# Optimization experiments

Measured on AMD Instinct MI355X. Metric: run time of the kernel, lower is better.

## Reference

```python
import jax, jax.numpy as jnp
import numpy as np

N = 50000
E = 800000
D = 128
EPS = 1e-12


def setup_inputs() -> dict:
    key = jax.random.key(0)
    ks = jax.random.split(key, 16)
    s = 1.0 / np.sqrt(D)
    inp = {
        "x": jax.random.normal(ks[0], (N, D), dtype=jnp.float32),
        "edge_src": jax.random.randint(ks[1], (E,), 0, N, dtype=jnp.int32),
        "edge_dst": jax.random.randint(ks[2], (E,), 0, N, dtype=jnp.int32),
    }
    names = ["Wpool0", "Wself0", "Wneigh0", "Wpool1", "Wself1", "Wneigh1"]
    for i, n in enumerate(names):
        inp[n] = jax.random.uniform(ks[3 + i], (D, D), dtype=jnp.float32, minval=-s, maxval=s)
    for i, n in enumerate(["bpool0", "b0", "bpool1", "b1"]):
        inp[n] = jax.random.uniform(ks[9 + i], (D,), dtype=jnp.float32, minval=-s, maxval=s)
    return inp


def _sage_pool(h, src, dst, Wpool, bpool, Wself, Wneigh, b):
    # per-neighbor transform: relu(fc_pool(h_src))
    m = jax.nn.relu(h @ Wpool.T + bpool)            # [N, D]
    # gather -> segment max over destination nodes (irregular access)
    agg = jax.ops.segment_max(m[src], dst, num_segments=N)  # [N, D], -inf for empty
    deg = jax.ops.segment_sum(jnp.ones((E,), jnp.float32), dst, num_segments=N)
    h_neigh = jnp.where(deg[:, None] > 0, agg, 0.0)  # DGL: zero for isolated nodes
    return h @ Wself.T + h_neigh @ Wneigh.T + b


def _l2norm(h):
    # torch F.normalize(dim=1, eps=1e-12)
    n = jnp.sqrt(jnp.sum(h * h, axis=1, keepdims=True))
    return h / jnp.maximum(n, EPS)


def reference(x, edge_src, edge_dst,
              Wpool0, Wself0, Wneigh0, Wpool1, Wself1, Wneigh1,
              bpool0, b0, bpool1, b1):
    # layer 0 (not last): conv -> relu -> normalize -> dropout(p=0)
    h = _sage_pool(x, edge_src, edge_dst, Wpool0, bpool0, Wself0, Wneigh0, b0)
    h = jax.nn.relu(h)
    h = _l2norm(h)
    enc_feat_input = h  # l == n_layers - 2
    # layer 1 (last): conv only
    h = _sage_pool(h, edge_src, edge_dst, Wpool1, bpool1, Wself1, Wneigh1, b1)
    return h, enc_feat_input
```

## Files before the change

kernel.cpp:

```cpp
#include <hip/hip_runtime.h>
#include <hip/hip_fp16.h>

#define DD 128
#define BK_SHIFT 6
#define BK_NODES 64
#define NBLK 256
#define SCAN_T 1024
#define SCAN_E 8
#define SCAN_CHUNK (SCAN_T * SCAN_E)

typedef __attribute__((ext_vector_type(8))) _Float16 f16x8;
typedef __attribute__((ext_vector_type(4))) float f32x4;

union h8u { f16x8 v; int i[4]; };

static __device__ __forceinline__ f16x8 vmax8(f16x8 a, f16x8 b) {
#pragma unroll
    for (int i = 0; i < 8; ++i) a[i] = a[i] > b[i] ? a[i] : b[i];
    return a;
}

__global__ void prep_w(const float* __restrict__ W0, const float* __restrict__ W1,
                       const float* __restrict__ W2, const float* __restrict__ W3,
                       const float* __restrict__ W4, const float* __restrict__ W5,
                       __half* __restrict__ Wh) {
    int idx = blockIdx.x * 256 + threadIdx.x;
    int wi = idx >> 14;
    int off = idx & 16383;
    int j = off >> 7;
    int k = off & 127;
    float a;
    switch (wi) {
        case 0: a = W0[off]; break;
        case 1: a = W1[off]; break;
        case 2: a = W2[off]; break;
        case 3: a = W3[off]; break;
        case 4: a = W4[off]; break;
        default: a = W5[off]; break;
    }
    int k2 = k ^ ((j & 7) << 3);
    Wh[(size_t)wi * 16384 + j * DD + k2] = __float2half(a);
}

__global__ void prep_x(const float* __restrict__ x, __half* __restrict__ xh, int n8) {
    int i = blockIdx.x * 256 + threadIdx.x;
    if (i >= n8) return;
    float4 u0 = *(const float4*)(x + (size_t)i * 8);
    float4 u1 = *(const float4*)(x + (size_t)i * 8 + 4);
    f16x8 v;
    v[0] = (_Float16)u0.x; v[1] = (_Float16)u0.y; v[2] = (_Float16)u0.z; v[3] = (_Float16)u0.w;
    v[4] = (_Float16)u1.x; v[5] = (_Float16)u1.y; v[6] = (_Float16)u1.z; v[7] = (_Float16)u1.w;
    *(f16x8*)(xh + (size_t)i * 8) = v;
}

__global__ __launch_bounds__(256) void hist2d_kernel(const int* __restrict__ dst,
                                                     int* __restrict__ hist2d,
                                                     int E, int NB, int chunk) {
    extern __shared__ int h[];
    int t = threadIdx.x, b = blockIdx.x;
    for (int i = t; i < NB; i += 256) h[i] = 0;
    __syncthreads();
    int e0 = b * chunk, e1 = min(e0 + chunk, E);
    for (int e = e0 + t; e < e1; e += 256)
        atomicAdd(&h[dst[e] >> BK_SHIFT], 1);
    __syncthreads();
    for (int i = t; i < NB; i += 256) hist2d[i * NBLK + b] = h[i];
}

__global__ __launch_bounds__(SCAN_T) void partial_reduce(const int* __restrict__ data,
                                                         int* __restrict__ bsum, int n) {
    __shared__ int s[SCAN_T];
    int t = threadIdx.x;
    int i0 = blockIdx.x * SCAN_CHUNK + t * SCAN_E;
    int sum = 0;
#pragma unroll
    for (int u = 0; u < SCAN_E; ++u) {
        int i = i0 + u;
        sum += (i < n) ? data[i] : 0;
    }
    s[t] = sum;
    __syncthreads();
    for (int off = SCAN_T / 2; off > 0; off >>= 1) {
        if (t < off) s[t] += s[t + off];
        __syncthreads();
    }
    if (t == 0) bsum[blockIdx.x] = s[0];
}

__global__ __launch_bounds__(SCAN_T) void scan_excl_inplace(int* __restrict__ data,
                                                            const int* __restrict__ bsum, int n) {
    __shared__ int s[SCAN_T];
    int t = threadIdx.x;
    int b = blockIdx.x;
    int carry = 0;
    for (int k = 0; k < b; ++k) carry += bsum[k];
    int i0 = b * SCAN_CHUNK + t * SCAN_E;
    int v[SCAN_E];
    int sum = 0;
#pragma unroll
    for (int u = 0; u < SCAN_E; ++u) {
        v[u] = (i0 + u < n) ? data[i0 + u] : 0;
        sum += v[u];
    }
    s[t] = sum;
    __syncthreads();
    for (int off = 1; off < SCAN_T; off <<= 1) {
        int x = (t >= off) ? s[t - off] : 0;
        __syncthreads();
        s[t] += x;
        __syncthreads();
    }
    int run = s[t] - sum + carry;
#pragma unroll
    for (int u = 0; u < SCAN_E; ++u) {
        int i = i0 + u;
        if (i < n) {
            data[i] = run;
            run += v[u];
        }
    }
}

__global__ __launch_bounds__(256) void bin_edges2(const int* __restrict__ src,
                                                  const int* __restrict__ dst,
                                                  const int* __restrict__ base,
                                                  unsigned* __restrict__ ebuf,
                                                  int E, int NB, int chunk) {
    extern __shared__ int h[];
    int t = threadIdx.x, b = blockIdx.x;
    for (int i = t; i < NB; i += 256) h[i] = base[i * NBLK + b];
    __syncthreads();
    int e0 = b * chunk, e1 = min(e0 + chunk, E);
    for (int e = e0 + t; e < e1; e += 256) {
        int d = dst[e];
        int p = atomicAdd(&h[d >> BK_SHIFT], 1);
        ebuf[p] = ((unsigned)src[e] << BK_SHIFT) | (unsigned)(d & (BK_NODES - 1));
    }
}

__global__ __launch_bounds__(256) void build_csr(const unsigned* __restrict__ ebuf,
                                                 const int* __restrict__ base,
                                                 int* __restrict__ rowptr,
                                                 int* __restrict__ csr_src, int N, int NB, int E) {
    __shared__ int cnt[BK_NODES];
    __shared__ int cur[BK_NODES];
    int b = blockIdx.x;
    int t = threadIdx.x;
    int beg = base[b * NBLK];
    int end = (b == NB - 1) ? E : base[(b + 1) * NBLK];
    if (b == 0 && t == 0) rowptr[0] = 0;
    if (t < BK_NODES) cnt[t] = 0;
    __syncthreads();
    for (int e = beg + t; e < end; e += 256)
        atomicAdd(&cnt[ebuf[e] & (BK_NODES - 1)], 1);
    __syncthreads();
    if (t < 64) {
        int v = cnt[t];
        int inc = v;
#pragma unroll
        for (int off = 1; off < 64; off <<= 1) {
            int x = __shfl_up(inc, off);
            if (t >= off) inc += x;
        }
        cur[t] = beg + inc - v;
        int node = b * BK_NODES + t;
        if (node < N) rowptr[node + 1] = beg + inc;
    }
    __syncthreads();
    for (int e = beg + t; e < end; e += 256) {
        unsigned v = ebuf[e];
        int p = atomicAdd(&cur[v & (BK_NODES - 1)], 1);
        csr_src[p] = (int)(v >> BK_SHIFT);
    }
}

__global__ __launch_bounds__(256) void segmax2(const __half* __restrict__ m,
                                               const int* __restrict__ rowptr,
                                               const int* __restrict__ csr_src,
                                               __half* __restrict__ agg, int n) {
    int node = blockIdx.x * 4 + (threadIdx.x >> 6);
    if (node >= n) return;
    int lane = threadIdx.x & 63;
    int g = lane >> 4;
    int l = lane & 15;
    int beg = rowptr[node], end = rowptr[node + 1];
    const __half* mp = m + l * 8;

    f16x8 acc0 = (f16x8)0, acc1 = (f16x8)0, acc2 = (f16x8)0, acc3 = (f16x8)0;

    int e = beg + g;
    for (; e + 12 < end; e += 16) {
        int s0 = csr_src[e];
        int s1 = csr_src[e + 4];
        int s2 = csr_src[e + 8];
        int s3 = csr_src[e + 12];
        f16x8 u0 = *(const f16x8*)(mp + (size_t)s0 * DD);
        f16x8 u1 = *(const f16x8*)(mp + (size_t)s1 * DD);
        f16x8 u2 = *(const f16x8*)(mp + (size_t)s2 * DD);
        f16x8 u3 = *(const f16x8*)(mp + (size_t)s3 * DD);
        acc0 = vmax8(acc0, u0);
        acc1 = vmax8(acc1, u1);
        acc2 = vmax8(acc2, u2);
        acc3 = vmax8(acc3, u3);
    }
    for (; e < end; e += 4) {
        int s0 = csr_src[e];
        f16x8 u0 = *(const f16x8*)(mp + (size_t)s0 * DD);
        acc0 = vmax8(acc0, u0);
    }

    h8u a;
    a.v = vmax8(vmax8(acc0, acc1), vmax8(acc2, acc3));
#pragma unroll
    for (int off = 16; off <= 32; off <<= 1) {
        h8u b;
#pragma unroll
        for (int c = 0; c < 4; ++c) b.i[c] = __shfl_xor(a.i[c], off);
        a.v = vmax8(a.v, b.v);
    }
    if (g == 0)
        *(f16x8*)(agg + (size_t)node * DD + l * 8) = a.v;
}

template <int EPI, bool FUSED>
__global__ __launch_bounds__(256) void gemm_f16(
    const __half* __restrict__ A,
    const __half* __restrict__ WA,
    const __half* __restrict__ G,
    const __half* __restrict__ WG,
    const float* __restrict__ bias,
    float* __restrict__ outf, __half* __restrict__ outh, int nrows) {
    __shared__ __half Ws[DD * DD];
    int tid = threadIdx.x;
    int lane = tid & 63;
    int w = tid >> 6;
    int l16 = lane & 15;
    int lg = lane >> 4;
    int rbase = blockIdx.x * 128 + w * 32;

    {
        const f32x4* src = (const f32x4*)(const void*)WA;
        f32x4* dst = (f32x4*)(void*)Ws;
#pragma unroll
        for (int i = 0; i < 8; ++i) dst[i * 256 + tid] = src[i * 256 + tid];
    }
    __syncthreads();

    int ar0 = min(rbase + l16, nrows - 1);
    int ar1 = min(rbase + 16 + l16, nrows - 1);
    size_t aoff0 = (size_t)ar0 * DD;
    size_t aoff1 = (size_t)ar1 * DD;

    f32x4 acc[2][8];
#pragma unroll
    for (int mt = 0; mt < 2; ++mt)
#pragma unroll
        for (int nt = 0; nt < 8; ++nt) acc[mt][nt] = (f32x4){0.f, 0.f, 0.f, 0.f};

    int swz = (l16 & 7) << 3;

#pragma unroll
    for (int kk = 0; kk < 4; ++kk) {
        int k0 = kk * 32 + lg * 8;
        f16x8 a0 = *(const f16x8*)(const void*)(A + aoff0 + k0);
        f16x8 a1 = *(const f16x8*)(const void*)(A + aoff1 + k0);
        int klds = k0 ^ swz;
#pragma unroll
        for (int nt = 0; nt < 8; ++nt) {
            f16x8 wh = *(const f16x8*)(const void*)(Ws + (nt * 16 + l16) * DD + klds);
            acc[0][nt] = __builtin_amdgcn_mfma_f32_16x16x32_f16(a0, wh, acc[0][nt], 0, 0, 0);
            acc[1][nt] = __builtin_amdgcn_mfma_f32_16x16x32_f16(a1, wh, acc[1][nt], 0, 0, 0);
        }
    }

    if constexpr (FUSED) {
        __syncthreads();
        {
            const f32x4* src = (const f32x4*)(const void*)WG;
            f32x4* dst = (f32x4*)(void*)Ws;
#pragma unroll
            for (int i = 0; i < 8; ++i) dst[i * 256 + tid] = src[i * 256 + tid];
        }
        __syncthreads();
#pragma unroll
        for (int kk = 0; kk < 4; ++kk) {
            int k0 = kk * 32 + lg * 8;
            f16x8 g0 = *(const f16x8*)(const void*)(G + aoff0 + k0);
            f16x8 g1 = *(const f16x8*)(const void*)(G + aoff1 + k0);
            int klds = k0 ^ swz;
#pragma unroll
            for (int nt = 0; nt < 8; ++nt) {
                f16x8 uh = *(const f16x8*)(const void*)(Ws + (nt * 16 + l16) * DD + klds);
                acc[0][nt] = __builtin_amdgcn_mfma_f32_16x16x32_f16(g0, uh, acc[0][nt], 0, 0, 0);
                acc[1][nt] = __builtin_amdgcn_mfma_f32_16x16x32_f16(g1, uh, acc[1][nt], 0, 0, 0);
            }
        }
    }

    float bv[8];
#pragma unroll
    for (int nt = 0; nt < 8; ++nt) bv[nt] = bias[nt * 16 + l16];

#pragma unroll
    for (int mt = 0; mt < 2; ++mt) {
#pragma unroll
        for (int r = 0; r < 4; ++r) {
            int row = rbase + mt * 16 + lg * 4 + r;
            float vv[8];
            float s = 0.f;
#pragma unroll
            for (int nt = 0; nt < 8; ++nt) {
                float v = acc[mt][nt][r] + bv[nt];
                if (EPI >= 1) v = fmaxf(v, 0.f);
                vv[nt] = v;
                s += v * v;
            }
            if constexpr (EPI == 2) {
                s += __shfl_xor(s, 1);
                s += __shfl_xor(s, 2);
                s += __shfl_xor(s, 4);
                s += __shfl_xor(s, 8);
                float sc = 1.0f / fmaxf(sqrtf(s), 1e-12f);
#pragma unroll
                for (int nt = 0; nt < 8; ++nt) vv[nt] *= sc;
            }
            if (row < nrows) {
                if constexpr (EPI == 1) {
#pragma unroll
                    for (int nt = 0; nt < 8; ++nt)
                        outh[(size_t)row * DD + nt * 16 + l16] = __float2half(vv[nt]);
                } else {
#pragma unroll
                    for (int nt = 0; nt < 8; ++nt)
                        outf[(size_t)row * DD + nt * 16 + l16] = vv[nt];
                    if (EPI == 2 && outh != nullptr) {
#pragma unroll
                        for (int nt = 0; nt < 8; ++nt)
                            outh[(size_t)row * DD + nt * 16 + l16] = __float2half(vv[nt]);
                    }
                }
            }
        }
    }
}

static inline size_t align16(size_t x) { return (x + 15) & ~(size_t)15; }

extern "C" void kernel_launch(void* const* d_in, const int* in_sizes, int n_in,
                              void* d_out, int out_size, void* d_ws, size_t ws_size,
                              hipStream_t stream) {
    const float* x  = (const float*)d_in[0];
    const int* esrc = (const int*)d_in[1];
    const int* edst = (const int*)d_in[2];
    const float* Wm[6];
    for (int i = 0; i < 6; ++i) Wm[i] = (const float*)d_in[3 + i];
    const float* bpool0 = (const float*)d_in[9];
    const float* b0     = (const float*)d_in[10];
    const float* bpool1 = (const float*)d_in[11];
    const float* b1     = (const float*)d_in[12];

    int N = in_sizes[0] / DD;
    int E = in_sizes[1];
    int NB = (N + BK_NODES - 1) >> BK_SHIFT;
    int chunk = (E + NBLK - 1) / NBLK;
    int nh = NB * NBLK;
    int nscan = (nh + SCAN_CHUNK - 1) / SCAN_CHUNK;

    char* p = (char*)d_ws;
    __half* Wh     = (__half*)p;   p += align16((size_t)6 * 16384 * 2);
    __half* xh     = (__half*)p;   p += align16((size_t)N * DD * 2);
    __half* ench   = (__half*)p;   p += align16((size_t)N * DD * 2);
    __half* m      = (__half*)p;   p += align16((size_t)N * DD * 2);
    __half* agg    = (__half*)p;   p += align16((size_t)N * DD * 2);
    int* hist2d    = (int*)p;      p += align16((size_t)nh * 4);
    int* bsum      = (int*)p;      p += align16((size_t)nscan * 4);
    int* rowptr    = (int*)p;      p += align16((size_t)(N + 1) * 4);
    unsigned* ebuf = (unsigned*)p; p += align16((size_t)E * 4);
    int* csr_src   = (int*)p;      p += align16((size_t)E * 4);

    float* out_h   = (float*)d_out;
    float* out_enc = (float*)d_out + (size_t)N * DD;

    prep_w<<<384, 256, 0, stream>>>(Wm[0], Wm[1], Wm[2], Wm[3], Wm[4], Wm[5], Wh);
    prep_x<<<(N * DD / 8 + 255) / 256, 256, 0, stream>>>(x, xh, N * DD / 8);
    hist2d_kernel<<<NBLK, 256, NB * 4, stream>>>(edst, hist2d, E, NB, chunk);
    partial_reduce<<<nscan, SCAN_T, 0, stream>>>(hist2d, bsum, nh);
    scan_excl_inplace<<<nscan, SCAN_T, 0, stream>>>(hist2d, bsum, nh);
    bin_edges2<<<NBLK, 256, NB * 4, stream>>>(esrc, edst, hist2d, ebuf, E, NB, chunk);
    build_csr<<<NB, 256, 0, stream>>>(ebuf, hist2d, rowptr, csr_src, N, NB, E);

    int gb = (N + 127) / 128;
    int sb = (N + 3) / 4;

    gemm_f16<1, false><<<gb, 256, 0, stream>>>(xh, Wh + 0 * 16384, nullptr, nullptr,
                                               bpool0, nullptr, m, N);
    segmax2<<<sb, 256, 0, stream>>>(m, rowptr, csr_src, agg, N);
    gemm_f16<2, true><<<gb, 256, 0, stream>>>(xh, Wh + 1 * 16384, agg, Wh + 2 * 16384,
                                              b0, out_enc, ench, N);

    gemm_f16<1, false><<<gb, 256, 0, stream>>>(ench, Wh + 3 * 16384, nullptr, nullptr,
                                               bpool1, nullptr, m, N);
    segmax2<<<sb, 256, 0, stream>>>(m, rowptr, csr_src, agg, N);
    gemm_f16<0, true><<<gb, 256, 0, stream>>>(ench, Wh + 4 * 16384, agg, Wh + 5 * 16384,
                                              b1, out_h, nullptr, N);
}
```

Before: 173.6 us.

## Split segment-max feature dimension across grid y into four 32-column slices

```diff
diff --git a/kernel.cpp b/kernel.cpp
--- a/kernel.cpp
+++ b/kernel.cpp
@@ -10,13 +10,14 @@
 #define SCAN_CHUNK (SCAN_T * SCAN_E)
 
 typedef __attribute__((ext_vector_type(8))) _Float16 f16x8;
+typedef __attribute__((ext_vector_type(2))) _Float16 f16x2;
 typedef __attribute__((ext_vector_type(4))) float f32x4;
 
-union h8u { f16x8 v; int i[4]; };
-
-static __device__ __forceinline__ f16x8 vmax8(f16x8 a, f16x8 b) {
-#pragma unroll
-    for (int i = 0; i < 8; ++i) a[i] = a[i] > b[i] ? a[i] : b[i];
+union h2u { f16x2 v; int i; };
+
+static __device__ __forceinline__ f16x2 vmax2(f16x2 a, f16x2 b) {
+    a[0] = a[0] > b[0] ? a[0] : b[0];
+    a[1] = a[1] > b[1] ? a[1] : b[1];
     return a;
 }
 
@@ -174,19 +175,20 @@
     }
 }
 
-__global__ __launch_bounds__(256) void segmax2(const __half* __restrict__ m,
-                                               const int* __restrict__ rowptr,
-                                               const int* __restrict__ csr_src,
-                                               __half* __restrict__ agg, int n) {
-    int node = blockIdx.x * 4 + (threadIdx.x >> 6);
+__global__ __launch_bounds__(1024) void segmax3(const __half* __restrict__ m,
+                                                const int* __restrict__ rowptr,
+                                                const int* __restrict__ csr_src,
+                                                __half* __restrict__ agg, int n) {
+    int node = blockIdx.x * 16 + (threadIdx.x >> 6);
     if (node >= n) return;
+    int q = blockIdx.y;
     int lane = threadIdx.x & 63;
     int g = lane >> 4;
     int l = lane & 15;
     int beg = rowptr[node], end = rowptr[node + 1];
-    const __half* mp = m + l * 8;
-
-    f16x8 acc0 = (f16x8)0, acc1 = (f16x8)0, acc2 = (f16x8)0, acc3 = (f16x8)0;
+    const __half* mp = m + q * 32 + l * 2;
+
+    f16x2 a0 = (f16x2)0, a1 = (f16x2)0, a2 = (f16x2)0, a3 = (f16x2)0;
 
     int e = beg + g;
     for (; e + 12 < end; e += 16) {
@@ -194,32 +196,31 @@
         int s1 = csr_src[e + 4];
         int s2 = csr_src[e + 8];
         int s3 = csr_src[e + 12];
-        f16x8 u0 = *(const f16x8*)(mp + (size_t)s0 * DD);
-        f16x8 u1 = *(const f16x8*)(mp + (size_t)s1 * DD);
-        f16x8 u2 = *(const f16x8*)(mp + (size_t)s2 * DD);
-        f16x8 u3 = *(const f16x8*)(mp + (size_t)s3 * DD);
-        acc0 = vmax8(acc0, u0);
-        acc1 = vmax8(acc1, u1);
-        acc2 = vmax8(acc2, u2);
-        acc3 = vmax8(acc3, u3);
+        f16x2 u0 = *(const f16x2*)(mp + (size_t)s0 * DD);
+        f16x2 u1 = *(const f16x2*)(mp + (size_t)s1 * DD);
+        f16x2 u2 = *(const f16x2*)(mp + (size_t)s2 * DD);
+        f16x2 u3 = *(const f16x2*)(mp + (size_t)s3 * DD);
+        a0 = vmax2(a0, u0);
+        a1 = vmax2(a1, u1);
+        a2 = vmax2(a2, u2);
+        a3 = vmax2(a3, u3);
     }
     for (; e < end; e += 4) {
         int s0 = csr_src[e];
-        f16x8 u0 = *(const f16x8*)(mp + (size_t)s0 * DD);
-        acc0 = vmax8(acc0, u0);
-    }
-
-    h8u a;
-    a.v = vmax8(vmax8(acc0, acc1), vmax8(acc2, acc3));
+        f16x2 u0 = *(const f16x2*)(mp + (size_t)s0 * DD);
+        a0 = vmax2(a0, u0);
+    }
+
+    h2u a;
+    a.v = vmax2(vmax2(a0, a1), vmax2(a2, a3));
 #pragma unroll
     for (int off = 16; off <= 32; off <<= 1) {
-        h8u b;
-#pragma unroll
-        for (int c = 0; c < 4; ++c) b.i[c] = __shfl_xor(a.i[c], off);
-        a.v = vmax8(a.v, b.v);
+        h2u b;
+        b.i = __shfl_xor(a.i, off);
+        a.v = vmax2(a.v, b.v);
     }
     if (g == 0)
-        *(f16x8*)(agg + (size_t)node * DD + l * 8) = a.v;
+        *(f16x2*)(agg + (size_t)node * DD + q * 32 + l * 2) = a.v;
 }
 
 template <int EPI, bool FUSED>
@@ -390,17 +391,17 @@
     build_csr<<<NB, 256, 0, stream>>>(ebuf, hist2d, rowptr, csr_src, N, NB, E);
 
     int gb = (N + 127) / 128;
-    int sb = (N + 3) / 4;
+    dim3 sg((N + 15) / 16, 4);
 
     gemm_f16<1, false><<<gb, 256, 0, stream>>>(xh, Wh + 0 * 16384, nullptr, nullptr,
                                                bpool0, nullptr, m, N);
-    segmax2<<<sb, 256, 0, stream>>>(m, rowptr, csr_src, agg, N);
+    segmax3<<<sg, 1024, 0, stream>>>(m, rowptr, csr_src, agg, N);
     gemm_f16<2, true><<<gb, 256, 0, stream>>>(xh, Wh + 1 * 16384, agg, Wh + 2 * 16384,
                                               b0, out_enc, ench, N);
 
     gemm_f16<1, false><<<gb, 256, 0, stream>>>(ench, Wh + 3 * 16384, nullptr, nullptr,
                                                bpool1, nullptr, m, N);
-    segmax2<<<sb, 256, 0, stream>>>(m, rowptr, csr_src, agg, N);
+    segmax3<<<sg, 1024, 0, stream>>>(m, rowptr, csr_src, agg, N);
     gemm_f16<0, true><<<gb, 256, 0, stream>>>(ench, Wh + 4 * 16384, agg, Wh + 5 * 16384,
                                               b1, out_h, nullptr, N);
 }
```

Measured after the change: 278.9 us. 60.6% more time.

## Split GEMM output columns across two wave groups with 512-thread blocks

Applied to the files above, without the earlier changes.

```diff
diff --git a/kernel.cpp b/kernel.cpp
--- a/kernel.cpp
+++ b/kernel.cpp
@@ -223,7 +223,7 @@
 }
 
 template <int EPI, bool FUSED>
-__global__ __launch_bounds__(256) void gemm_f16(
+__global__ __launch_bounds__(512) void gemm_f16(
     const __half* __restrict__ A,
     const __half* __restrict__ WA,
     const __half* __restrict__ G,
@@ -231,18 +231,22 @@
     const float* __restrict__ bias,
     float* __restrict__ outf, __half* __restrict__ outh, int nrows) {
     __shared__ __half Ws[DD * DD];
+    __shared__ float pbuf[2][DD];
     int tid = threadIdx.x;
     int lane = tid & 63;
     int w = tid >> 6;
     int l16 = lane & 15;
     int lg = lane >> 4;
-    int rbase = blockIdx.x * 128 + w * 32;
+    int ch = w >> 2;
+    int wr = w & 3;
+    int blk0 = blockIdx.x * 128;
+    int rbase = blk0 + wr * 32;
 
     {
         const f32x4* src = (const f32x4*)(const void*)WA;
         f32x4* dst = (f32x4*)(void*)Ws;
 #pragma unroll
-        for (int i = 0; i < 8; ++i) dst[i * 256 + tid] = src[i * 256 + tid];
+        for (int i = 0; i < 4; ++i) dst[i * 512 + tid] = src[i * 512 + tid];
     }
     __syncthreads();
 
@@ -251,11 +255,11 @@
     size_t aoff0 = (size_t)ar0 * DD;
     size_t aoff1 = (size_t)ar1 * DD;
 
-    f32x4 acc[2][8];
+    f32x4 acc[2][4];
 #pragma unroll
     for (int mt = 0; mt < 2; ++mt)
 #pragma unroll
-        for (int nt = 0; nt < 8; ++nt) acc[mt][nt] = (f32x4){0.f, 0.f, 0.f, 0.f};
+        for (int nt = 0; nt < 4; ++nt) acc[mt][nt] = (f32x4){0.f, 0.f, 0.f, 0.f};
 
     int swz = (l16 & 7) << 3;
 
@@ -266,8 +270,8 @@
         f16x8 a1 = *(const f16x8*)(const void*)(A + aoff1 + k0);
         int klds = k0 ^ swz;
 #pragma unroll
-        for (int nt = 0; nt < 8; ++nt) {
-            f16x8 wh = *(const f16x8*)(const void*)(Ws + (nt * 16 + l16) * DD + klds);
+        for (int nt = 0; nt < 4; ++nt) {
+            f16x8 wh = *(const f16x8*)(const void*)(Ws + (ch * 64 + nt * 16 + l16) * DD + klds);
             acc[0][nt] = __builtin_amdgcn_mfma_f32_16x16x32_f16(a0, wh, acc[0][nt], 0, 0, 0);
             acc[1][nt] = __builtin_amdgcn_mfma_f32_16x16x32_f16(a1, wh, acc[1][nt], 0, 0, 0);
         }
@@ -279,7 +283,7 @@
             const f32x4* src = (const f32x4*)(const void*)WG;
             f32x4* dst = (f32x4*)(void*)Ws;
 #pragma unroll
-            for (int i = 0; i < 8; ++i) dst[i * 256 + tid] = src[i * 256 + tid];
+            for (int i = 0; i < 4; ++i) dst[i * 512 + tid] = src[i * 512 + tid];
         }
         __syncthreads();
 #pragma unroll
@@ -289,55 +293,70 @@
             f16x8 g1 = *(const f16x8*)(const void*)(G + aoff1 + k0);
             int klds = k0 ^ swz;
 #pragma unroll
-            for (int nt = 0; nt < 8; ++nt) {
-                f16x8 uh = *(const f16x8*)(const void*)(Ws + (nt * 16 + l16) * DD + klds);
+            for (int nt = 0; nt < 4; ++nt) {
+                f16x8 uh = *(const f16x8*)(const void*)(Ws + (ch * 64 + nt * 16 + l16) * DD + klds);
                 acc[0][nt] = __builtin_amdgcn_mfma_f32_16x16x32_f16(g0, uh, acc[0][nt], 0, 0, 0);
                 acc[1][nt] = __builtin_amdgcn_mfma_f32_16x16x32_f16(g1, uh, acc[1][nt], 0, 0, 0);
             }
         }
     }
 
-    float bv[8];
-#pragma unroll
-    for (int nt = 0; nt < 8; ++nt) bv[nt] = bias[nt * 16 + l16];
-
-#pragma unroll
-    for (int mt = 0; mt < 2; ++mt) {
-#pragma unroll
-        for (int r = 0; r < 4; ++r) {
-            int row = rbase + mt * 16 + lg * 4 + r;
-            float vv[8];
-            float s = 0.f;
-#pragma unroll
-            for (int nt = 0; nt < 8; ++nt) {
-                float v = acc[mt][nt][r] + bv[nt];
-                if (EPI >= 1) v = fmaxf(v, 0.f);
-                vv[nt] = v;
-                s += v * v;
-            }
-            if constexpr (EPI == 2) {
+    float bv[4];
+#pragma unroll
+    for (int nt = 0; nt < 4; ++nt) bv[nt] = bias[ch * 64 + nt * 16 + l16];
+
+    if constexpr (EPI == 2) {
+#pragma unroll
+        for (int mt = 0; mt < 2; ++mt) {
+#pragma unroll
+            for (int r = 0; r < 4; ++r) {
+                float s = 0.f;
+#pragma unroll
+                for (int nt = 0; nt < 4; ++nt) {
+                    float v = fmaxf(acc[mt][nt][r] + bv[nt], 0.f);
+                    s += v * v;
+                }
                 s += __shfl_xor(s, 1);
                 s += __shfl_xor(s, 2);
                 s += __shfl_xor(s, 4);
                 s += __shfl_xor(s, 8);
-                float sc = 1.0f / fmaxf(sqrtf(s), 1e-12f);
-#pragma unroll
-                for (int nt = 0; nt < 8; ++nt) vv[nt] *= sc;
+                if (l16 == 0) pbuf[ch][wr * 32 + mt * 16 + lg * 4 + r] = s;
             }
-            if (row < nrows) {
-                if constexpr (EPI == 1) {
-#pragma unroll
-                    for (int nt = 0; nt < 8; ++nt)
-                        outh[(size_t)row * DD + nt * 16 + l16] = __float2half(vv[nt]);
-                } else {
-#pragma unroll
-                    for (int nt = 0; nt < 8; ++nt)
-                        outf[(size_t)row * DD + nt * 16 + l16] = vv[nt];
-                    if (EPI == 2 && outh != nullptr) {
-#pragma unroll
-                        for (int nt = 0; nt < 8; ++nt)
-                            outh[(size_t)row * DD + nt * 16 + l16] = __float2half(vv[nt]);
+        }
+        __syncthreads();
+#pragma unroll
+        for (int mt = 0; mt < 2; ++mt) {
+#pragma unroll
+            for (int r = 0; r < 4; ++r) {
+                int lrow = wr * 32 + mt * 16 + lg * 4 + r;
+                int row = blk0 + lrow;
+                float tot = pbuf[0][lrow] + pbuf[1][lrow];
+                float sc = 1.0f / fmaxf(sqrtf(tot), 1e-12f);
+                if (row < nrows) {
+#pragma unroll
+                    for (int nt = 0; nt < 4; ++nt) {
+                        float v = fmaxf(acc[mt][nt][r] + bv[nt], 0.f) * sc;
+                        size_t o = (size_t)row * DD + ch * 64 + nt * 16 + l16;
+                        outf[o] = v;
+                        outh[o] = __float2half(v);
                     }
+                }
+            }
+        }
+    } else {
+#pragma unroll
+        for (int mt = 0; mt < 2; ++mt) {
+#pragma unroll
+            for (int r = 0; r < 4; ++r) {
+                int row = rbase + mt * 16 + lg * 4 + r;
+                if (row >= nrows) continue;
+#pragma unroll
+                for (int nt = 0; nt < 4; ++nt) {
+                    float v = acc[mt][nt][r] + bv[nt];
+                    if (EPI == 1) v = fmaxf(v, 0.f);
+                    size_t o = (size_t)row * DD + ch * 64 + nt * 16 + l16;
+                    if constexpr (EPI == 1) outh[o] = __float2half(v);
+                    else                    outf[o] = v;
                 }
             }
         }
@@ -392,15 +411,15 @@
     int gb = (N + 127) / 128;
     int sb = (N + 3) / 4;
 
-    gemm_f16<1, false><<<gb, 256, 0, stream>>>(xh, Wh + 0 * 16384, nullptr, nullptr,
+    gemm_f16<1, false><<<gb, 512, 0, stream>>>(xh, Wh + 0 * 16384, nullptr, nullptr,
                                                bpool0, nullptr, m, N);
     segmax2<<<sb, 256, 0, stream>>>(m, rowptr, csr_src, agg, N);
-    gemm_f16<2, true><<<gb, 256, 0, stream>>>(xh, Wh + 1 * 16384, agg, Wh + 2 * 16384,
+    gemm_f16<2, true><<<gb, 512, 0, stream>>>(xh, Wh + 1 * 16384, agg, Wh + 2 * 16384,
                                               b0, out_enc, ench, N);
 
-    gemm_f16<1, false><<<gb, 256, 0, stream>>>(ench, Wh + 3 * 16384, nullptr, nullptr,
+    gemm_f16<1, false><<<gb, 512, 0, stream>>>(ench, Wh + 3 * 16384, nullptr, nullptr,
                                                bpool1, nullptr, m, N);
     segmax2<<<sb, 256, 0, stream>>>(m, rowptr, csr_src, agg, N);
-    gemm_f16<0, true><<<gb, 256, 0, stream>>>(ench, Wh + 4 * 16384, agg, Wh + 5 * 16384,
+    gemm_f16<0, true><<<gb, 512, 0, stream>>>(ench, Wh + 4 * 16384, agg, Wh + 5 * 16384,
                                               b1, out_h, nullptr, N);
 }
```

Result: no change. 176.1 us (+1.4%).

## Pre-sort edges by source bucket before destination binning for gather locality

Applied to the files above, without the earlier changes.

```diff
diff --git a/kernel.cpp b/kernel.cpp
--- a/kernel.cpp
+++ b/kernel.cpp
@@ -53,7 +53,7 @@
     *(f16x8*)(xh + (size_t)i * 8) = v;
 }
 
-__global__ __launch_bounds__(256) void hist2d_kernel(const int* __restrict__ dst,
+__global__ __launch_bounds__(256) void hist2d_kernel(const int* __restrict__ key,
                                                      int* __restrict__ hist2d,
                                                      int E, int NB, int chunk) {
     extern __shared__ int h[];
@@ -62,7 +62,7 @@
     __syncthreads();
     int e0 = b * chunk, e1 = min(e0 + chunk, E);
     for (int e = e0 + t; e < e1; e += 256)
-        atomicAdd(&h[dst[e] >> BK_SHIFT], 1);
+        atomicAdd(&h[key[e] >> BK_SHIFT], 1);
     __syncthreads();
     for (int i = t; i < NB; i += 256) hist2d[i * NBLK + b] = h[i];
 }
@@ -118,6 +118,24 @@
             data[i] = run;
             run += v[u];
         }
+    }
+}
+
+__global__ __launch_bounds__(256) void bin_src(const int* __restrict__ src,
+                                               const int* __restrict__ dst,
+                                               const int* __restrict__ base,
+                                               int* __restrict__ es2, int* __restrict__ ed2,
+                                               int E, int NB, int chunk) {
+    extern __shared__ int h[];
+    int t = threadIdx.x, b = blockIdx.x;
+    for (int i = t; i < NB; i += 256) h[i] = base[i * NBLK + b];
+    __syncthreads();
+    int e0 = b * chunk, e1 = min(e0 + chunk, E);
+    for (int e = e0 + t; e < e1; e += 256) {
+        int s = src[e];
+        int p = atomicAdd(&h[s >> BK_SHIFT], 1);
+        es2[p] = s;
+        ed2[p] = dst[e];
     }
 }
 
@@ -372,9 +390,12 @@
     __half* ench   = (__half*)p;   p += align16((size_t)N * DD * 2);
     __half* m      = (__half*)p;   p += align16((size_t)N * DD * 2);
     __half* agg    = (__half*)p;   p += align16((size_t)N * DD * 2);
-    int* hist2d    = (int*)p;      p += align16((size_t)nh * 4);
+    int* hist2dA   = (int*)p;      p += align16((size_t)nh * 4);
+    int* hist2dB   = (int*)p;      p += align16((size_t)nh * 4);
     int* bsum      = (int*)p;      p += align16((size_t)nscan * 4);
     int* rowptr    = (int*)p;      p += align16((size_t)(N + 1) * 4);
+    int* es2       = (int*)p;      p += align16((size_t)E * 4);
+    int* ed2       = (int*)p;      p += align16((size_t)E * 4);
     unsigned* ebuf = (unsigned*)p; p += align16((size_t)E * 4);
     int* csr_src   = (int*)p;      p += align16((size_t)E * 4);
 
@@ -383,11 +404,17 @@
 
     prep_w<<<384, 256, 0, stream>>>(Wm[0], Wm[1], Wm[2], Wm[3], Wm[4], Wm[5], Wh);
     prep_x<<<(N * DD / 8 + 255) / 256, 256, 0, stream>>>(x, xh, N * DD / 8);
-    hist2d_kernel<<<NBLK, 256, NB * 4, stream>>>(edst, hist2d, E, NB, chunk);
-    partial_reduce<<<nscan, SCAN_T, 0, stream>>>(hist2d, bsum, nh);
-    scan_excl_inplace<<<nscan, SCAN_T, 0, stream>>>(hist2d, bsum, nh);
-    bin_edges2<<<NBLK, 256, NB * 4, stream>>>(esrc, edst, hist2d, ebuf, E, NB, chunk);
-    build_csr<<<NB, 256, 0, stream>>>(ebuf, hist2d, rowptr, csr_src, N, NB, E);
+
+    hist2d_kernel<<<NBLK, 256, NB * 4, stream>>>(esrc, hist2dA, E, NB, chunk);
+    partial_reduce<<<nscan, SCAN_T, 0, stream>>>(hist2dA, bsum, nh);
+    scan_excl_inplace<<<nscan, SCAN_T, 0, stream>>>(hist2dA, bsum, nh);
+    bin_src<<<NBLK, 256, NB * 4, stream>>>(esrc, edst, hist2dA, es2, ed2, E, NB, chunk);
+
+    hist2d_kernel<<<NBLK, 256, NB * 4, stream>>>(ed2, hist2dB, E, NB, chunk);
+    partial_reduce<<<nscan, SCAN_T, 0, stream>>>(hist2dB, bsum, nh);
+    scan_excl_inplace<<<nscan, SCAN_T, 0, stream>>>(hist2dB, bsum, nh);
+    bin_edges2<<<NBLK, 256, NB * 4, stream>>>(es2, ed2, hist2dB, ebuf, E, NB, chunk);
+    build_csr<<<NB, 256, 0, stream>>>(ebuf, hist2dB, rowptr, csr_src, N, NB, E);
 
     int gb = (N + 127) / 128;
     int sb = (N + 3) / 4;
```

New measurement: 216.1 us. +24.5%, slower.
